# Kernel optimization log

Measured on AMD Instinct MI355X. Metric: run time of the kernel, lower is better.

The kernel has to match this reference:

```python
import jax, jax.numpy as jnp
import numpy as np

B, T, N, H, F, E = 8, 64, 2048, 64, 64, 32768
G = 3 * H  # GRU gate dim


def setup_inputs() -> dict:
    key = jax.random.key(0)
    ks = jax.random.split(key, 12)
    s = 0.05
    return {
        "x": jax.random.normal(ks[0], (B, T, N, F), jnp.float32),
        "targets": jax.random.normal(ks[1], (B, T, N, 1), jnp.float32),
        "targets_mask": jax.random.uniform(ks[2], (B, T, N, 1)) > 0.2,
        "edge_index": jax.random.randint(ks[3], (2, E), 0, N),
        "W_msg": jax.random.normal(ks[4], (H, H), jnp.float32) * s,
        "b_msg": jnp.zeros((H,), jnp.float32),
        "W_mix": jax.random.normal(ks[5], (H, H + F), jnp.float32) * s,
        "b_mix": jnp.zeros((H,), jnp.float32),
        "W_ih": jax.random.normal(ks[6], (N, G, H), jnp.float32) * s,
        "W_hh": jax.random.normal(ks[7], (N, G, H), jnp.float32) * s,
        "b_ih": jnp.zeros((N, G), jnp.float32),
        "b_hh": jnp.zeros((N, G), jnp.float32),
        "W_read": jax.random.normal(ks[8], (1, H), jnp.float32) * s,
        "b_read": jnp.zeros((1,), jnp.float32),
    }


def reference(x, targets, targets_mask, edge_index,
              W_msg, b_msg, W_mix, b_mix,
              W_ih, W_hh, b_ih, b_hh, W_read, b_read):
    src, dst = edge_index[0], edge_index[1]

    def step(state, x_t):
        # state: [B,N,H], x_t: [B,N,F]
        m = jnp.einsum('bnh,gh->bng', state, W_msg) + b_msg           # state_to_message
        agg = jnp.zeros_like(m).at[:, dst, :].add(m[:, src, :])       # add-aggregate over directed edges
        mi = jnp.concatenate([agg, x_t], axis=-1)                     # [B,N,H+F]
        m2 = jnp.einsum('bnf,hf->bnh', mi, W_mix) + b_mix             # mix_input
        # per-node independent GRU cells (batched weights [N,3H,*])
        gi = jnp.einsum('bnh,ngh->bng', m2, W_ih) + b_ih
        gh = jnp.einsum('bnh,ngh->bng', state, W_hh) + b_hh
        i_r, i_z, i_n = jnp.split(gi, 3, axis=-1)
        h_r, h_z, h_n = jnp.split(gh, 3, axis=-1)
        r = jax.nn.sigmoid(i_r + h_r)
        z = jax.nn.sigmoid(i_z + h_z)
        n_cand = jnp.tanh(i_n + r * h_n)
        new_state = (1.0 - z) * n_cand + z * state
        out = jnp.einsum('bnh,oh->bno', new_state, W_read) + b_read   # readout -> [B,N,1]
        return new_state, out

    state0 = jnp.zeros((B, N, H), x.dtype)
    _, outs = jax.lax.scan(step, state0, jnp.swapaxes(x, 0, 1))       # outs: [T,B,N,1]
    outputs = jnp.swapaxes(outs, 0, 1)                                # [B,T,N,1]
    loss = 0.5 * (outputs - targets) ** 2
    mask = targets_mask.astype(loss.dtype)
    return jnp.sum(loss * mask) / jnp.sum(mask)                       # masked mean
```

## Files before the change

kernel.cpp:

```cpp
#include <hip/hip_runtime.h>
#include <math.h>

namespace {
constexpr int B = 8, T = 64, N = 2048, H = 64, F = 64, E = 32768, G = 192;
constexpr int BNH = B * N * H;
constexpr int NWELEM = N * G * H;
}

typedef __attribute__((ext_vector_type(8))) short bfrag;
typedef __attribute__((ext_vector_type(4))) float ffrag;
typedef long f8frag;

#define MFMA(a, b, c)  __builtin_amdgcn_mfma_f32_16x16x32_bf16(a, b, c, 0, 0, 0)
#define MFMA8(a, b, c) __builtin_amdgcn_mfma_f32_16x16x32_fp8_fp8(a, b, c, 0, 0, 0)

#define DS (1.f / 512.f)

__device__ __forceinline__ unsigned short f2bf(float f) {
  unsigned u = __float_as_uint(f);
  u += 0x7fffu + ((u >> 16) & 1u);
  return (unsigned short)(u >> 16);
}
__device__ __forceinline__ float bf2f(unsigned short u) {
  return __uint_as_float(((unsigned)u) << 16);
}
template<bool HI>
__device__ __forceinline__ unsigned cvtpk8(float a, float b, unsigned old) {
  return __builtin_amdgcn_cvt_pk_fp8_f32(a, b, old, HI);
}


__global__ __launch_bounds__(256) void init_kernel(
    float* __restrict__ state, unsigned short* __restrict__ mA,
    const float* __restrict__ b_msg, float* __restrict__ loss_acc,
    float* __restrict__ scal, int* __restrict__ deg)
{
  int stride = gridDim.x * blockDim.x;
  for (int i = blockIdx.x * blockDim.x + threadIdx.x; i < BNH; i += stride) {
    state[i] = 0.f;
    mA[i] = f2bf(b_msg[i & (H - 1)]);
    if (i < N) { loss_acc[i] = 0.f; deg[i] = 0; }
    if (i < 16) scal[i] = 0.f;
  }
}

__global__ __launch_bounds__(256) void conv_kernel(
    const float* __restrict__ Wi, const float* __restrict__ Wh,
    const float* __restrict__ Wm, const float* __restrict__ Wg,
    unsigned char* __restrict__ Wib, unsigned char* __restrict__ Whb,
    unsigned short* __restrict__ Wmb, unsigned short* __restrict__ Wgb)
{
  int stride = gridDim.x * blockDim.x * 2;
  for (int i = (blockIdx.x * blockDim.x + threadIdx.x) * 2; i < NWELEM; i += stride) {
    unsigned p = cvtpk8<false>(Wi[i] * 32.f, Wi[i + 1] * 32.f, 0u);
    *(unsigned short*)(Wib + i) = (unsigned short)p;
    p = cvtpk8<false>(Wh[i] * 32.f, Wh[i + 1] * 32.f, 0u);
    *(unsigned short*)(Whb + i) = (unsigned short)p;
    if (i < 64 * 128) { Wmb[i] = f2bf(Wm[i]); Wmb[i + 1] = f2bf(Wm[i + 1]); }
    if (i < 64 * 64)  { Wgb[i] = f2bf(Wg[i]); Wgb[i + 1] = f2bf(Wg[i + 1]); }
  }
}

__global__ __launch_bounds__(256) void hist_kernel(const int* __restrict__ ei, int* __restrict__ deg) {
  int e = blockIdx.x * 256 + threadIdx.x;
  if (e < E) atomicAdd(&deg[ei[E + e]], 1);
}

__global__ __launch_bounds__(1024) void scan_kernel(const int* __restrict__ deg,
    int* __restrict__ row_ptr, int* __restrict__ cursor)
{
  __shared__ int s[N];
  int tid = threadIdx.x;
  s[tid] = deg[tid];
  s[tid + 1024] = deg[tid + 1024];
  __syncthreads();
  for (int off = 1; off < N; off <<= 1) {
    int v0 = (tid >= off) ? s[tid - off] : 0;
    int v1 = s[tid + 1024 - off];
    __syncthreads();
    s[tid] += v0;
    s[tid + 1024] += v1;
    __syncthreads();
  }
  row_ptr[tid + 1] = s[tid];
  row_ptr[tid + 1025] = s[tid + 1024];
  cursor[tid] = (tid == 0) ? 0 : s[tid - 1];
  cursor[tid + 1024] = s[tid + 1023];
  if (tid == 0) row_ptr[0] = 0;
}

__global__ __launch_bounds__(256) void fill_kernel(const int* __restrict__ ei,
    int* __restrict__ cursor, int* __restrict__ col_src)
{
  int e = blockIdx.x * 256 + threadIdx.x;
  if (e < E) {
    int d = ei[E + e];
    int slot = atomicAdd(&cursor[d], 1);
    col_src[slot] = ei[e];
  }
}

__global__ __launch_bounds__(256) void mask_kernel(const int* __restrict__ mask, float* __restrict__ scal) {
  int stride = gridDim.x * blockDim.x;
  int v = 0;
  for (int i = blockIdx.x * blockDim.x + threadIdx.x; i < B * T * N; i += stride)
    v += (mask[i] != 0);
  for (int o = 1; o < 64; o <<= 1) v += __shfl_xor(v, o, 64);
  if ((threadIdx.x & 63) == 0) atomicAdd(&scal[0], (float)v);
}


__global__ __launch_bounds__(256, 4) void step_kernel(
    const float* __restrict__ x, const float* __restrict__ targets,
    const int* __restrict__ mask, float* __restrict__ state,
    const unsigned char* __restrict__ W_ihb, const unsigned char* __restrict__ W_hhb,
    const unsigned short* __restrict__ W_mixb, const unsigned short* __restrict__ W_msgb,
    const float* __restrict__ b_ih, const float* __restrict__ b_hh,
    const float* __restrict__ b_mix, const float* __restrict__ b_msg,
    const float* __restrict__ W_read, const float* __restrict__ b_read,
    const int* __restrict__ row_ptr, const int* __restrict__ col_src,
    const unsigned short* __restrict__ m_cur, unsigned short* __restrict__ m_nxt,
    float* __restrict__ loss_acc, int t)
{
  __shared__ float partial[4][8][72];
  __shared__ unsigned char m2F8[8 * 80];
  __shared__ unsigned short nsA[8 * 72];
  __shared__ float redS[4][8];

  const int n = blockIdx.x;
  const int tid = threadIdx.x;
  const int w = tid >> 6, lane = tid & 63;
  const int mrow = lane & 15, quad = lane >> 4;
  const bfrag za = (bfrag)0;

  f8frag whf[6];
  {
    const unsigned char* Wh = W_hhb + (size_t)n * (G * H);
#pragma unroll
    for (int tt = 0; tt < 3; ++tt) {
      const unsigned char* wrh = Wh + (((w + tt * 4) * 16 + mrow) * H) + quad * 8;
      whf[2 * tt]     = *(const f8frag*)(wrh);
      whf[2 * tt + 1] = *(const f8frag*)(wrh + 32);
    }
  }
  f8frag asF0 = 0, asF1 = 0;
  float4 xv0 = {0.f,0.f,0.f,0.f}, xv1 = {0.f,0.f,0.f,0.f};
  float4 xv2 = {0.f,0.f,0.f,0.f}, xv3 = {0.f,0.f,0.f,0.f};
  if (mrow < 8) {
    const float* sp = state + (size_t)n * (B * H) + mrow * H;
    float4 s0 = *(const float4*)(sp + quad * 8);
    float4 s1 = *(const float4*)(sp + quad * 8 + 4);
    float4 s2 = *(const float4*)(sp + 32 + quad * 8);
    float4 s3 = *(const float4*)(sp + 32 + quad * 8 + 4);
    unsigned u0 = 0, u1 = 0;
    u0 = cvtpk8<false>(s0.x * 16.f, s0.y * 16.f, u0);
    u0 = cvtpk8<true>(s0.z * 16.f, s0.w * 16.f, u0);
    u1 = cvtpk8<false>(s1.x * 16.f, s1.y * 16.f, u1);
    u1 = cvtpk8<true>(s1.z * 16.f, s1.w * 16.f, u1);
    asF0 = (f8frag)(((unsigned long long)u1 << 32) | u0);
    u0 = 0; u1 = 0;
    u0 = cvtpk8<false>(s2.x * 16.f, s2.y * 16.f, u0);
    u0 = cvtpk8<true>(s2.z * 16.f, s2.w * 16.f, u0);
    u1 = cvtpk8<false>(s3.x * 16.f, s3.y * 16.f, u1);
    u1 = cvtpk8<true>(s3.z * 16.f, s3.w * 16.f, u1);
    asF1 = (f8frag)(((unsigned long long)u1 << 32) | u0);
    const float* xp = x + (((size_t)mrow * T + t) * N + n) * F;
    xv0 = *(const float4*)(xp + quad * 8);
    xv1 = *(const float4*)(xp + quad * 8 + 4);
    xv2 = *(const float4*)(xp + 32 + quad * 8);
    xv3 = *(const float4*)(xp + 32 + quad * 8 + 4);
  }
  {
    float acc[8] = {0.f,0.f,0.f,0.f,0.f,0.f,0.f,0.f};
    const int e0 = row_ptr[n], e1 = row_ptr[n + 1];
#pragma unroll 2
    for (int e = e0 + w; e < e1; e += 4) {
      const unsigned short* mp = m_cur + (size_t)col_src[e] * (B * H) + lane;
#pragma unroll
      for (int b = 0; b < 8; ++b) acc[b] += bf2f(mp[b * H]);
    }
#pragma unroll
    for (int b = 0; b < 8; ++b) partial[w][b][lane] = acc[b];
  }
  ffrag ah0 = {0.f,0.f,0.f,0.f}, ah1 = {0.f,0.f,0.f,0.f}, ah2 = {0.f,0.f,0.f,0.f};
  ah0 = MFMA8(asF0, whf[0], ah0); ah0 = MFMA8(asF1, whf[1], ah0);
  ah1 = MFMA8(asF0, whf[2], ah1); ah1 = MFMA8(asF1, whf[3], ah1);
  ah2 = MFMA8(asF0, whf[4], ah2); ah2 = MFMA8(asF1, whf[5], ah2);
  __syncthreads();

  f8frag wif[6];
  {
    const unsigned char* Wi = W_ihb + (size_t)n * (G * H);
#pragma unroll
    for (int tt = 0; tt < 3; ++tt) {
      const unsigned char* wri = Wi + (((w + tt * 4) * 16 + mrow) * H) + quad * 8;
      wif[2 * tt]     = *(const f8frag*)(wri);
      wif[2 * tt + 1] = *(const f8frag*)(wri + 32);
    }
  }
  {
    const int g0 = w * 16;
    bfrag a0 = za, a1 = za, a2 = za, a3 = za;
    if (mrow < 8) {
      const float* p = &partial[0][mrow][quad * 8];
#pragma unroll
      for (int j = 0; j < 8; ++j) {
        float s = p[j] + p[j + 576] + p[j + 1152] + p[j + 1728];
        a0[j] = (short)f2bf(s);
      }
      const float* p2 = &partial[0][mrow][32 + quad * 8];
#pragma unroll
      for (int j = 0; j < 8; ++j) {
        float s = p2[j] + p2[j + 576] + p2[j + 1152] + p2[j + 1728];
        a1[j] = (short)f2bf(s);
      }
      a2[0]=(short)f2bf(xv0.x); a2[1]=(short)f2bf(xv0.y); a2[2]=(short)f2bf(xv0.z); a2[3]=(short)f2bf(xv0.w);
      a2[4]=(short)f2bf(xv1.x); a2[5]=(short)f2bf(xv1.y); a2[6]=(short)f2bf(xv1.z); a2[7]=(short)f2bf(xv1.w);
      a3[0]=(short)f2bf(xv2.x); a3[1]=(short)f2bf(xv2.y); a3[2]=(short)f2bf(xv2.z); a3[3]=(short)f2bf(xv2.w);
      a3[4]=(short)f2bf(xv3.x); a3[5]=(short)f2bf(xv3.y); a3[6]=(short)f2bf(xv3.z); a3[7]=(short)f2bf(xv3.w);
    }
    const unsigned short* wm = W_mixb + (g0 + mrow) * 128 + quad * 8;
    ffrag accm = {0.f, 0.f, 0.f, 0.f};
    accm = MFMA(a0, *(const bfrag*)(wm), accm);
    accm = MFMA(a1, *(const bfrag*)(wm + 32), accm);
    accm = MFMA(a2, *(const bfrag*)(wm + 64), accm);
    accm = MFMA(a3, *(const bfrag*)(wm + 96), accm);
    if (quad < 2) {
      float bm = b_mix[g0 + mrow];
#pragma unroll
      for (int r = 0; r < 4; ++r) {
        unsigned p = cvtpk8<false>((accm[r] + bm) * 16.f, 0.f, 0u);
        m2F8[(quad * 4 + r) * 80 + g0 + mrow] = (unsigned char)(p & 0xffu);
      }
    }
  }
  __syncthreads();

  {
    f8frag amF0 = 0, amF1 = 0;
    if (mrow < 8) {
      amF0 = *(const f8frag*)&m2F8[mrow * 80 + quad * 8];
      amF1 = *(const f8frag*)&m2F8[mrow * 80 + 32 + quad * 8];
    }
    ffrag ai0 = {0.f,0.f,0.f,0.f}, ai1 = {0.f,0.f,0.f,0.f}, ai2 = {0.f,0.f,0.f,0.f};
    ai0 = MFMA8(amF0, wif[0], ai0); ai0 = MFMA8(amF1, wif[1], ai0);
    ai1 = MFMA8(amF0, wif[2], ai1); ai1 = MFMA8(amF1, wif[3], ai1);
    ai2 = MFMA8(amF0, wif[4], ai2); ai2 = MFMA8(amF1, wif[5], ai2);
    if (quad < 2) {
      const int hcol = w * 16 + mrow;
      const int bg = n * G + hcol;
      const float bir = b_ih[bg], biz = b_ih[bg + 64], bin_ = b_ih[bg + 128];
      const float bhr = b_hh[bg], bhz = b_hh[bg + 64], bhn = b_hh[bg + 128];
      const float wrd = W_read[hcol];
      float v[4];
#pragma unroll
      for (int r = 0; r < 4; ++r) {
        const int b = quad * 4 + r;
        float rs  = (ai0[r] + ah0[r]) * DS + bir + bhr;
        float zs  = (ai1[r] + ah1[r]) * DS + biz + bhz;
        float in_ = ai2[r] * DS + bin_;
        float hn  = ah2[r] * DS + bhn;
        float rg = 1.f / (1.f + __expf(-rs));
        float z  = 1.f / (1.f + __expf(-zs));
        float pre = in_ + rg * hn;
        float a = __expf(-2.f * fabsf(pre));
        float nc = copysignf((1.f - a) / (1.f + a), pre);
        float sold = state[(size_t)n * (B * H) + b * H + hcol];
        float ns = (1.f - z) * nc + z * sold;
        state[(size_t)n * (B * H) + b * H + hcol] = ns;
        nsA[b * 72 + hcol] = f2bf(ns);
        v[r] = ns * wrd;
      }
#pragma unroll
      for (int o = 1; o < 16; o <<= 1) {
#pragma unroll
        for (int r = 0; r < 4; ++r) v[r] += __shfl_xor(v[r], o, 64);
      }
      if (mrow == 0) {
#pragma unroll
        for (int r = 0; r < 4; ++r) redS[w][quad * 4 + r] = v[r];
      }
    }
  }
  __syncthreads();

  {
    const int g0 = w * 16;
    bfrag an0 = za, an1 = za;
    if (mrow < 8) {
      an0 = *(const bfrag*)&nsA[mrow * 72 + quad * 8];
      an1 = *(const bfrag*)&nsA[mrow * 72 + 32 + quad * 8];
    }
    const unsigned short* wg = W_msgb + (g0 + mrow) * H + quad * 8;
    ffrag accg = {0.f, 0.f, 0.f, 0.f};
    accg = MFMA(an0, *(const bfrag*)(wg), accg);
    accg = MFMA(an1, *(const bfrag*)(wg + 32), accg);
    if (quad < 2) {
      float bm = b_msg[g0 + mrow];
#pragma unroll
      for (int r = 0; r < 4; ++r)
        m_nxt[(size_t)n * (B * H) + (quad * 4 + r) * H + g0 + mrow] = f2bf(accg[r] + bm);
    }
  }
  if (tid < 8) {
    float vv = redS[0][tid] + redS[1][tid] + redS[2][tid] + redS[3][tid] + b_read[0];
    size_t idx = ((size_t)tid * T + t) * N + n;
    float d = vv - targets[idx];
    float l = (mask[idx] != 0) ? 0.5f * d * d : 0.f;
    l += __shfl_xor(l, 1, 64);
    l += __shfl_xor(l, 2, 64);
    l += __shfl_xor(l, 4, 64);
    if (tid == 0) loss_acc[n] += l;
  }
}

__global__ __launch_bounds__(256) void final_kernel(const float* __restrict__ loss_acc,
    const float* __restrict__ scal, float* __restrict__ out)
{
  __shared__ float sred[4];
  float v = 0.f;
  for (int i = threadIdx.x; i < N; i += 256) v += loss_acc[i];
  for (int o = 1; o < 64; o <<= 1) v += __shfl_xor(v, o, 64);
  if ((threadIdx.x & 63) == 0) sred[threadIdx.x >> 6] = v;
  __syncthreads();
  if (threadIdx.x == 0) out[0] = (sred[0] + sred[1] + sred[2] + sred[3]) / scal[0];
}

extern "C" void kernel_launch(void* const* d_in, const int* in_sizes, int n_in,
                              void* d_out, int out_size, void* d_ws, size_t ws_size,
                              hipStream_t stream)
{
  const float* x       = (const float*)d_in[0];
  const float* targets = (const float*)d_in[1];
  const int*   mask    = (const int*)d_in[2];
  const int*   ei      = (const int*)d_in[3];
  const float* W_msg   = (const float*)d_in[4];
  const float* b_msg   = (const float*)d_in[5];
  const float* W_mix   = (const float*)d_in[6];
  const float* b_mix   = (const float*)d_in[7];
  const float* W_ih    = (const float*)d_in[8];
  const float* W_hh    = (const float*)d_in[9];
  const float* b_ih    = (const float*)d_in[10];
  const float* b_hh    = (const float*)d_in[11];
  const float* W_read  = (const float*)d_in[12];
  const float* b_read  = (const float*)d_in[13];
  float* out = (float*)d_out;

  float* state          = (float*)d_ws;
  unsigned short* mA    = (unsigned short*)(state + BNH);
  unsigned short* mB    = mA + BNH;
  float* loss_acc       = (float*)(mB + BNH);
  float* scal           = loss_acc + N;
  int* deg              = (int*)(scal + 16);
  int* row_ptr          = deg + N;
  int* cursor           = row_ptr + (N + 16);
  int* col_src          = cursor + N;
  unsigned char* W_ihb  = (unsigned char*)(col_src + E);
  unsigned char* W_hhb  = W_ihb + NWELEM;
  unsigned short* W_mixb = (unsigned short*)(W_hhb + NWELEM);
  unsigned short* W_msgb = W_mixb + 64 * 128;

  init_kernel<<<1024, 256, 0, stream>>>(state, mA, b_msg, loss_acc, scal, deg);
  conv_kernel<<<8192, 256, 0, stream>>>(W_ih, W_hh, W_mix, W_msg, W_ihb, W_hhb, W_mixb, W_msgb);
  hist_kernel<<<E / 256, 256, 0, stream>>>(ei, deg);
  scan_kernel<<<1, 1024, 0, stream>>>(deg, row_ptr, cursor);
  fill_kernel<<<E / 256, 256, 0, stream>>>(ei, cursor, col_src);
  mask_kernel<<<512, 256, 0, stream>>>(mask, scal);

  unsigned short* mcur = mA;
  unsigned short* mnxt = mB;
  for (int t = 0; t < T; ++t) {
    step_kernel<<<N, 256, 0, stream>>>(x, targets, mask, state,
                                       W_ihb, W_hhb, W_mixb, W_msgb,
                                       b_ih, b_hh, b_mix, b_msg, W_read, b_read,
                                       row_ptr, col_src, mcur, mnxt, loss_acc, t);
    unsigned short* tmp = mcur; mcur = mnxt; mnxt = tmp;
  }
  final_kernel<<<1, 256, 0, stream>>>(loss_acc, scal, out);
}
```

Measured before the change: 2.222 ms.

## Replace per-timestep launches with persistent kernel using grid barrier

```diff
diff --git a/kernel.cpp b/kernel.cpp
--- a/kernel.cpp
+++ b/kernel.cpp
@@ -5,6 +5,7 @@
 constexpr int B = 8, T = 64, N = 2048, H = 64, F = 64, E = 32768, G = 192;
 constexpr int BNH = B * N * H;
 constexpr int NWELEM = N * G * H;
+constexpr int NBLK = 1024;
 }
 
 typedef __attribute__((ext_vector_type(8))) short bfrag;
@@ -29,16 +30,36 @@
   return __builtin_amdgcn_cvt_pk_fp8_f32(a, b, old, HI);
 }
 
+__device__ __forceinline__ void grid_bar(int* bar, int t) {
+  __syncthreads();
+  if (threadIdx.x == 0) {
+    __threadfence();
+    int old = __hip_atomic_fetch_add(&bar[(blockIdx.x & 63) * 64], 1,
+                                     __ATOMIC_RELAXED, __HIP_MEMORY_SCOPE_AGENT);
+    if ((old & 15) == 15) {
+      int old2 = __hip_atomic_fetch_add(&bar[4096], 1,
+                                        __ATOMIC_RELAXED, __HIP_MEMORY_SCOPE_AGENT);
+      if ((old2 & 63) == 63)
+        __hip_atomic_fetch_add(&bar[4160], 1, __ATOMIC_RELAXED, __HIP_MEMORY_SCOPE_AGENT);
+    }
+    while (__hip_atomic_load(&bar[4160], __ATOMIC_RELAXED, __HIP_MEMORY_SCOPE_AGENT) <= t)
+      __builtin_amdgcn_s_sleep(8);
+    __threadfence();
+  }
+  __syncthreads();
+}
+
 
 __global__ __launch_bounds__(256) void init_kernel(
     float* __restrict__ state, unsigned short* __restrict__ mA,
     const float* __restrict__ b_msg, float* __restrict__ loss_acc,
-    float* __restrict__ scal, int* __restrict__ deg)
+    float* __restrict__ scal, int* __restrict__ deg, int* __restrict__ bar)
 {
   int stride = gridDim.x * blockDim.x;
   for (int i = blockIdx.x * blockDim.x + threadIdx.x; i < BNH; i += stride) {
     state[i] = 0.f;
     mA[i] = f2bf(b_msg[i & (H - 1)]);
+    if (i < 8192) bar[i] = 0;
     if (i < N) { loss_acc[i] = 0.f; deg[i] = 0; }
     if (i < 16) scal[i] = 0.f;
   }
@@ -107,6 +128,240 @@
     v += (mask[i] != 0);
   for (int o = 1; o < 64; o <<= 1) v += __shfl_xor(v, o, 64);
   if ((threadIdx.x & 63) == 0) atomicAdd(&scal[0], (float)v);
+}
+
+
+__global__ __launch_bounds__(256, 4) void persist_kernel(
+    const float* __restrict__ x, const float* __restrict__ targets,
+    const int* __restrict__ mask,
+    const unsigned char* __restrict__ W_ihb, const unsigned char* __restrict__ W_hhb,
+    const unsigned short* __restrict__ W_mixb, const unsigned short* __restrict__ W_msgb,
+    const float* __restrict__ b_ih, const float* __restrict__ b_hh,
+    const float* __restrict__ b_mix, const float* __restrict__ b_msg,
+    const float* __restrict__ W_read, const float* __restrict__ b_read,
+    const int* __restrict__ row_ptr, const int* __restrict__ col_src,
+    unsigned short* __restrict__ mAb, unsigned short* __restrict__ mBb,
+    float* __restrict__ loss_acc, int* __restrict__ bar)
+{
+  __shared__ float sts[2][8][64];
+  __shared__ float partial[4][8][72];
+  __shared__ unsigned char m2F8[8 * 80];
+  __shared__ unsigned short nsA[8 * 72];
+  __shared__ float redS[4][8];
+
+  const int tid = threadIdx.x;
+  const int w = tid >> 6, lane = tid & 63;
+  const int mrow = lane & 15, quad = lane >> 4;
+  const int n0 = blockIdx.x * 2;
+  const bfrag za = (bfrag)0;
+  const int hcol = w * 16 + mrow;
+
+  f8frag whf[2][6], wif[2][6];
+#pragma unroll
+  for (int k = 0; k < 2; ++k) {
+    const unsigned char* Wh = W_hhb + (size_t)(n0 + k) * (G * H);
+    const unsigned char* Wi = W_ihb + (size_t)(n0 + k) * (G * H);
+#pragma unroll
+    for (int tt = 0; tt < 3; ++tt) {
+      const int off = ((w + tt * 4) * 16 + mrow) * H + quad * 8;
+      whf[k][2 * tt]     = *(const f8frag*)(Wh + off);
+      whf[k][2 * tt + 1] = *(const f8frag*)(Wh + off + 32);
+      wif[k][2 * tt]     = *(const f8frag*)(Wi + off);
+      wif[k][2 * tt + 1] = *(const f8frag*)(Wi + off + 32);
+    }
+  }
+  const unsigned short* wmp = W_mixb + hcol * 128 + quad * 8;
+  const bfrag wm0 = *(const bfrag*)(wmp);
+  const bfrag wm1 = *(const bfrag*)(wmp + 32);
+  const bfrag wm2 = *(const bfrag*)(wmp + 64);
+  const bfrag wm3 = *(const bfrag*)(wmp + 96);
+  const unsigned short* wgp = W_msgb + hcol * H + quad * 8;
+  const bfrag wg0 = *(const bfrag*)(wgp);
+  const bfrag wg1 = *(const bfrag*)(wgp + 32);
+
+  float bir[2], biz[2], bin_[2], bhr[2], bhz[2], bhn[2];
+#pragma unroll
+  for (int k = 0; k < 2; ++k) {
+    const int bg = (n0 + k) * G + hcol;
+    bir[k] = b_ih[bg]; biz[k] = b_ih[bg + 64]; bin_[k] = b_ih[bg + 128];
+    bhr[k] = b_hh[bg]; bhz[k] = b_hh[bg + 64]; bhn[k] = b_hh[bg + 128];
+  }
+  const float wrd = W_read[hcol];
+  const float bmix = b_mix[hcol];
+  const float bmsg = b_msg[hcol];
+  const float brd = b_read[0];
+  const int e0a = row_ptr[n0], e0b = row_ptr[n0 + 1], e0c = row_ptr[n0 + 2];
+
+  for (int i = tid; i < 2 * 8 * 64; i += 256) ((float*)sts)[i] = 0.f;
+  __syncthreads();
+
+  float lsum[2] = {0.f, 0.f};
+  unsigned short* mcur = mAb;
+  unsigned short* mnxt = mBb;
+
+#pragma unroll 1
+  for (int t = 0; t < T; ++t) {
+#pragma unroll
+    for (int k = 0; k < 2; ++k) {
+      const int nn = n0 + k;
+      const int ee0 = k ? e0b : e0a;
+      const int ee1 = k ? e0c : e0b;
+
+      f8frag asF0 = 0, asF1 = 0;
+      bfrag a2 = za, a3 = za;
+      if (mrow < 8) {
+        const float* sp = &sts[k][mrow][0];
+        {
+          float4 s0 = *(const float4*)(sp + quad * 8);
+          float4 s1 = *(const float4*)(sp + quad * 8 + 4);
+          unsigned u0 = 0, u1 = 0;
+          u0 = cvtpk8<false>(s0.x * 16.f, s0.y * 16.f, u0);
+          u0 = cvtpk8<true >(s0.z * 16.f, s0.w * 16.f, u0);
+          u1 = cvtpk8<false>(s1.x * 16.f, s1.y * 16.f, u1);
+          u1 = cvtpk8<true >(s1.z * 16.f, s1.w * 16.f, u1);
+          asF0 = (f8frag)(((unsigned long long)u1 << 32) | u0);
+          s0 = *(const float4*)(sp + 32 + quad * 8);
+          s1 = *(const float4*)(sp + 32 + quad * 8 + 4);
+          u0 = 0; u1 = 0;
+          u0 = cvtpk8<false>(s0.x * 16.f, s0.y * 16.f, u0);
+          u0 = cvtpk8<true >(s0.z * 16.f, s0.w * 16.f, u0);
+          u1 = cvtpk8<false>(s1.x * 16.f, s1.y * 16.f, u1);
+          u1 = cvtpk8<true >(s1.z * 16.f, s1.w * 16.f, u1);
+          asF1 = (f8frag)(((unsigned long long)u1 << 32) | u0);
+        }
+        const float* xp = x + (((size_t)mrow * T + t) * N + nn) * F;
+        {
+          float4 t0 = *(const float4*)(xp + quad * 8);
+          float4 t1 = *(const float4*)(xp + quad * 8 + 4);
+          a2[0]=(short)f2bf(t0.x); a2[1]=(short)f2bf(t0.y); a2[2]=(short)f2bf(t0.z); a2[3]=(short)f2bf(t0.w);
+          a2[4]=(short)f2bf(t1.x); a2[5]=(short)f2bf(t1.y); a2[6]=(short)f2bf(t1.z); a2[7]=(short)f2bf(t1.w);
+          t0 = *(const float4*)(xp + 32 + quad * 8);
+          t1 = *(const float4*)(xp + 32 + quad * 8 + 4);
+          a3[0]=(short)f2bf(t0.x); a3[1]=(short)f2bf(t0.y); a3[2]=(short)f2bf(t0.z); a3[3]=(short)f2bf(t0.w);
+          a3[4]=(short)f2bf(t1.x); a3[5]=(short)f2bf(t1.y); a3[6]=(short)f2bf(t1.z); a3[7]=(short)f2bf(t1.w);
+        }
+      }
+      {
+        float acc[8] = {0.f,0.f,0.f,0.f,0.f,0.f,0.f,0.f};
+#pragma unroll 2
+        for (int e = ee0 + w; e < ee1; e += 4) {
+          const unsigned short* mp = mcur + (size_t)col_src[e] * (B * H) + lane;
+#pragma unroll
+          for (int b = 0; b < 8; ++b) acc[b] += bf2f(mp[b * H]);
+        }
+#pragma unroll
+        for (int b = 0; b < 8; ++b) partial[w][b][lane] = acc[b];
+      }
+      ffrag ah0 = {0.f,0.f,0.f,0.f}, ah1 = {0.f,0.f,0.f,0.f}, ah2 = {0.f,0.f,0.f,0.f};
+      ah0 = MFMA8(asF0, whf[k][0], ah0); ah0 = MFMA8(asF1, whf[k][1], ah0);
+      ah1 = MFMA8(asF0, whf[k][2], ah1); ah1 = MFMA8(asF1, whf[k][3], ah1);
+      ah2 = MFMA8(asF0, whf[k][4], ah2); ah2 = MFMA8(asF1, whf[k][5], ah2);
+      __syncthreads();
+
+      {
+        bfrag a0 = za, a1 = za;
+        if (mrow < 8) {
+          const float* p = &partial[0][mrow][quad * 8];
+#pragma unroll
+          for (int j = 0; j < 8; ++j) {
+            float s = p[j] + p[j + 576] + p[j + 1152] + p[j + 1728];
+            a0[j] = (short)f2bf(s);
+          }
+          const float* p2 = &partial[0][mrow][32 + quad * 8];
+#pragma unroll
+          for (int j = 0; j < 8; ++j) {
+            float s = p2[j] + p2[j + 576] + p2[j + 1152] + p2[j + 1728];
+            a1[j] = (short)f2bf(s);
+          }
+        }
+        ffrag accm = {0.f, 0.f, 0.f, 0.f};
+        accm = MFMA(a0, wm0, accm);
+        accm = MFMA(a1, wm1, accm);
+        accm = MFMA(a2, wm2, accm);
+        accm = MFMA(a3, wm3, accm);
+        if (quad < 2) {
+#pragma unroll
+          for (int r = 0; r < 4; ++r) {
+            unsigned p = cvtpk8<false>((accm[r] + bmix) * 16.f, 0.f, 0u);
+            m2F8[(quad * 4 + r) * 80 + hcol] = (unsigned char)(p & 0xffu);
+          }
+        }
+      }
+      __syncthreads();
+
+      {
+        f8frag amF0 = 0, amF1 = 0;
+        if (mrow < 8) {
+          amF0 = *(const f8frag*)&m2F8[mrow * 80 + quad * 8];
+          amF1 = *(const f8frag*)&m2F8[mrow * 80 + 32 + quad * 8];
+        }
+        ffrag ai0 = {0.f,0.f,0.f,0.f}, ai1 = {0.f,0.f,0.f,0.f}, ai2 = {0.f,0.f,0.f,0.f};
+        ai0 = MFMA8(amF0, wif[k][0], ai0); ai0 = MFMA8(amF1, wif[k][1], ai0);
+        ai1 = MFMA8(amF0, wif[k][2], ai1); ai1 = MFMA8(amF1, wif[k][3], ai1);
+        ai2 = MFMA8(amF0, wif[k][4], ai2); ai2 = MFMA8(amF1, wif[k][5], ai2);
+        if (quad < 2) {
+          float v[4];
+#pragma unroll
+          for (int r = 0; r < 4; ++r) {
+            const int b = quad * 4 + r;
+            float rs  = (ai0[r] + ah0[r]) * DS + bir[k] + bhr[k];
+            float zs  = (ai1[r] + ah1[r]) * DS + biz[k] + bhz[k];
+            float in_ = ai2[r] * DS + bin_[k];
+            float hn  = ah2[r] * DS + bhn[k];
+            float rg = 1.f / (1.f + __expf(-rs));
+            float z  = 1.f / (1.f + __expf(-zs));
+            float pre = in_ + rg * hn;
+            float a = __expf(-2.f * fabsf(pre));
+            float nc = copysignf((1.f - a) / (1.f + a), pre);
+            float sold = sts[k][b][hcol];
+            float ns = (1.f - z) * nc + z * sold;
+            sts[k][b][hcol] = ns;
+            nsA[b * 72 + hcol] = f2bf(ns);
+            v[r] = ns * wrd;
+          }
+#pragma unroll
+          for (int o = 1; o < 16; o <<= 1) {
+#pragma unroll
+            for (int r = 0; r < 4; ++r) v[r] += __shfl_xor(v[r], o, 64);
+          }
+          if (mrow == 0) {
+#pragma unroll
+            for (int r = 0; r < 4; ++r) redS[w][quad * 4 + r] = v[r];
+          }
+        }
+      }
+      __syncthreads();
+
+      {
+        bfrag an0 = za, an1 = za;
+        if (mrow < 8) {
+          an0 = *(const bfrag*)&nsA[mrow * 72 + quad * 8];
+          an1 = *(const bfrag*)&nsA[mrow * 72 + 32 + quad * 8];
+        }
+        ffrag accg = {0.f, 0.f, 0.f, 0.f};
+        accg = MFMA(an0, wg0, accg);
+        accg = MFMA(an1, wg1, accg);
+        if (quad < 2) {
+#pragma unroll
+          for (int r = 0; r < 4; ++r)
+            mnxt[(size_t)nn * (B * H) + (quad * 4 + r) * H + hcol] = f2bf(accg[r] + bmsg);
+        }
+      }
+      if (tid < 8) {
+        float vv = redS[0][tid] + redS[1][tid] + redS[2][tid] + redS[3][tid] + brd;
+        size_t idx = ((size_t)tid * T + t) * N + nn;
+        float d = vv - targets[idx];
+        float l = (mask[idx] != 0) ? 0.5f * d * d : 0.f;
+        l += __shfl_xor(l, 1, 64);
+        l += __shfl_xor(l, 2, 64);
+        l += __shfl_xor(l, 4, 64);
+        if (tid == 0) lsum[k] += l;
+      }
+    }
+    grid_bar(bar, t);
+    unsigned short* tp = mcur; mcur = mnxt; mnxt = tp;
+  }
+  if (tid == 0) { loss_acc[n0] = lsum[0]; loss_acc[n0 + 1] = lsum[1]; }
 }
 
 
@@ -154,15 +409,15 @@
     float4 s3 = *(const float4*)(sp + 32 + quad * 8 + 4);
     unsigned u0 = 0, u1 = 0;
     u0 = cvtpk8<false>(s0.x * 16.f, s0.y * 16.f, u0);
-    u0 = cvtpk8<true>(s0.z * 16.f, s0.w * 16.f, u0);
+    u0 = cvtpk8<true >(s0.z * 16.f, s0.w * 16.f, u0);
     u1 = cvtpk8<false>(s1.x * 16.f, s1.y * 16.f, u1);
-    u1 = cvtpk8<true>(s1.z * 16.f, s1.w * 16.f, u1);
+    u1 = cvtpk8<true >(s1.z * 16.f, s1.w * 16.f, u1);
     asF0 = (f8frag)(((unsigned long long)u1 << 32) | u0);
     u0 = 0; u1 = 0;
     u0 = cvtpk8<false>(s2.x * 16.f, s2.y * 16.f, u0);
-    u0 = cvtpk8<true>(s2.z * 16.f, s2.w * 16.f, u0);
+    u0 = cvtpk8<true >(s2.z * 16.f, s2.w * 16.f, u0);
     u1 = cvtpk8<false>(s3.x * 16.f, s3.y * 16.f, u1);
-    u1 = cvtpk8<true>(s3.z * 16.f, s3.w * 16.f, u1);
+    u1 = cvtpk8<true >(s3.z * 16.f, s3.w * 16.f, u1);
     asF1 = (f8frag)(((unsigned long long)u1 << 32) | u0);
     const float* xp = x + (((size_t)mrow * T + t) * N + n) * F;
     xv0 = *(const float4*)(xp + quad * 8);
@@ -355,26 +610,40 @@
   int* row_ptr          = deg + N;
   int* cursor           = row_ptr + (N + 16);
   int* col_src          = cursor + N;
-  unsigned char* W_ihb  = (unsigned char*)(col_src + E);
+  int* bar              = col_src + E;
+  unsigned char* W_ihb  = (unsigned char*)(bar + 8192);
   unsigned char* W_hhb  = W_ihb + NWELEM;
   unsigned short* W_mixb = (unsigned short*)(W_hhb + NWELEM);
   unsigned short* W_msgb = W_mixb + 64 * 128;
 
-  init_kernel<<<1024, 256, 0, stream>>>(state, mA, b_msg, loss_acc, scal, deg);
+  init_kernel<<<1024, 256, 0, stream>>>(state, mA, b_msg, loss_acc, scal, deg, bar);
   conv_kernel<<<8192, 256, 0, stream>>>(W_ih, W_hh, W_mix, W_msg, W_ihb, W_hhb, W_mixb, W_msgb);
   hist_kernel<<<E / 256, 256, 0, stream>>>(ei, deg);
   scan_kernel<<<1, 1024, 0, stream>>>(deg, row_ptr, cursor);
   fill_kernel<<<E / 256, 256, 0, stream>>>(ei, cursor, col_src);
   mask_kernel<<<512, 256, 0, stream>>>(mask, scal);
 
-  unsigned short* mcur = mA;
-  unsigned short* mnxt = mB;
-  for (int t = 0; t < T; ++t) {
-    step_kernel<<<N, 256, 0, stream>>>(x, targets, mask, state,
-                                       W_ihb, W_hhb, W_mixb, W_msgb,
-                                       b_ih, b_hh, b_mix, b_msg, W_read, b_read,
-                                       row_ptr, col_src, mcur, mnxt, loss_acc, t);
-    unsigned short* tmp = mcur; mcur = mnxt; mnxt = tmp;
+  int dev = 0, ncu = 0, occ = 0;
+  hipGetDevice(&dev);
+  hipDeviceGetAttribute(&ncu, hipDeviceAttributeMultiprocessorCount, dev);
+  hipOccupancyMaxActiveBlocksPerMultiprocessor(&occ, (const void*)persist_kernel, 256, 0);
+  const bool use_persist = ((long)occ * ncu >= NBLK);
+
+  if (use_persist) {
+    persist_kernel<<<NBLK, 256, 0, stream>>>(x, targets, mask,
+                                             W_ihb, W_hhb, W_mixb, W_msgb,
+                                             b_ih, b_hh, b_mix, b_msg, W_read, b_read,
+                                             row_ptr, col_src, mA, mB, loss_acc, bar);
+  } else {
+    unsigned short* mcur = mA;
+    unsigned short* mnxt = mB;
+    for (int t = 0; t < T; ++t) {
+      step_kernel<<<N, 256, 0, stream>>>(x, targets, mask, state,
+                                         W_ihb, W_hhb, W_mixb, W_msgb,
+                                         b_ih, b_hh, b_mix, b_msg, W_read, b_read,
+                                         row_ptr, col_src, mcur, mnxt, loss_acc, t);
+      unsigned short* tmp = mcur; mcur = mnxt; mnxt = tmp;
+    }
   }
   final_kernel<<<1, 256, 0, stream>>>(loss_acc, scal, out);
 }
```

Result: no change. 2.220 ms (-0.1%).
